# Kernel optimization log

Hardware: AMD Instinct MI355X
Metric: run time of the kernel (lower is better)

Reference implementation:

```python
import jax, jax.numpy as jnp
import numpy as np

N = 50000
E = 1600000
D_IN = 128
D_H = 128
D_OUT = 128
R = 2


def setup_inputs() -> dict:
    key = jax.random.key(0)
    ks = jax.random.split(key, 12)
    s = 0.02
    return {
        "x": jax.random.normal(ks[0], (N, D_IN), dtype=jnp.float32),
        "edge_index": jax.random.randint(ks[1], (2, E), 0, N, dtype=jnp.int64),
        "enc_w1": jax.random.normal(ks[2], (D_IN, D_H), dtype=jnp.float32) * s,
        "enc_b1": jnp.zeros((D_H,), dtype=jnp.float32),
        "enc_w2": jax.random.normal(ks[3], (D_H, D_H), dtype=jnp.float32) * s,
        "enc_b2": jnp.zeros((D_H,), dtype=jnp.float32),
        "comm_w": jax.random.normal(ks[4], (R, D_H, D_H), dtype=jnp.float32) * s,
        "comm_b": jnp.zeros((R, D_H), dtype=jnp.float32),
        "dec_w1": jax.random.normal(ks[5], (D_H, D_H), dtype=jnp.float32) * s,
        "dec_b1": jnp.zeros((D_H,), dtype=jnp.float32),
        "dec_w2": jax.random.normal(ks[6], (D_H, D_OUT), dtype=jnp.float32) * s,
        "dec_b2": jnp.zeros((D_OUT,), dtype=jnp.float32),
    }


def _segment_mean_messages(h, src, dst):
    # message[i] = mean over edges with source i of h[dst]; zeros if no neighbors
    gathered = h[dst]                                   # [E, D_H]
    sums = jax.ops.segment_sum(gathered, src, num_segments=N)   # [N, D_H]
    cnt = jax.ops.segment_sum(jnp.ones((src.shape[0],), h.dtype), src, num_segments=N)
    return sums / jnp.maximum(cnt, 1.0)[:, None]


def reference(x, edge_index, enc_w1, enc_b1, enc_w2, enc_b2,
              comm_w, comm_b, dec_w1, dec_b1, dec_w2, dec_b2):
    src, dst = edge_index[0], edge_index[1]
    # encoder: Linear -> ReLU -> Linear
    h = jax.nn.relu(x @ enc_w1 + enc_b1) @ enc_w2 + enc_b2
    # communication rounds
    for r in range(comm_w.shape[0]):
        msg = _segment_mean_messages(h, src, dst)       # [N, D_H]
        h = h + jax.nn.relu(msg @ comm_w[r] + comm_b[r])
    # decoder: Linear -> ReLU -> Linear
    return jax.nn.relu(h @ dec_w1 + dec_b1) @ dec_w2 + dec_b2
```

## Files before the change

### kernel.cpp

```cpp
#include <hip/hip_runtime.h>

#define NN 50000
#define EE 1600000
#define D 128
#define EPB 16384
#define NBIN ((EE + EPB - 1) / EPB)
#define NBKT 196
#define CAP 160
#define REC_CAP 12544

typedef __attribute__((ext_vector_type(8))) short bf16x8;
typedef __attribute__((ext_vector_type(4))) float f32x4;

static __device__ __forceinline__ unsigned short f2bf(float f) {
  unsigned u = __float_as_uint(f);
  u += 0x7fffu + ((u >> 16) & 1u);
  return (unsigned short)(u >> 16);
}
static __device__ __forceinline__ float bf2f(unsigned short s) {
  return __uint_as_float(((unsigned)s) << 16);
}

__global__ __launch_bounds__(256) void wt_prep(const float* __restrict__ ew1,
                                               const float* __restrict__ ew2,
                                               const float* __restrict__ cw,
                                               const float* __restrict__ dw1,
                                               const float* __restrict__ dw2,
                                               unsigned short* __restrict__ wt) {
  const int m = blockIdx.x;
  const float* W = (m == 0) ? ew1 : (m == 1) ? ew2 : (m == 2) ? cw
                 : (m == 3) ? (cw + 16384) : (m == 4) ? dw1 : dw2;
  unsigned short* o = wt + m * 16384;
  for (int i = threadIdx.x; i < 16384; i += 256) {
    const int col = i >> 7, k = i & 127;
    o[i] = f2bf(W[k * D + col]);
  }
}

__global__ __launch_bounds__(1024) void bin_edges(const int* __restrict__ src,
                                                  const int* __restrict__ dst,
                                                  unsigned* __restrict__ fifo_raw,
                                                  int* __restrict__ lcnt_g, int E) {
  __shared__ int lcnt[NBKT];
  const int t = threadIdx.x;
  for (int i = t; i < NBKT; i += 1024) lcnt[i] = 0;
  __syncthreads();
  const int base = blockIdx.x * EPB;
  #pragma unroll
  for (int it = 0; it < EPB / 1024; ++it) {
    const int e = base + it * 1024 + t;
    if (e < E) {
      const int s = src[e];
      const int d = dst[e];
      const int b = s >> 8;
      const int slot = atomicAdd(&lcnt[b], 1);
      if (slot < CAP)
        fifo_raw[((size_t)blockIdx.x * NBKT + b) * CAP + slot] =
            (unsigned)(s & 255) | ((unsigned)d << 8);
    }
  }
  __syncthreads();
  for (int i = t; i < NBKT; i += 1024)
    lcnt_g[blockIdx.x * NBKT + i] = min(lcnt[i], CAP);
}

__global__ __launch_bounds__(128) void seg_scan(const int* __restrict__ lcnt_g,
                                                int* __restrict__ seg_loc,
                                                int* __restrict__ btot) {
  __shared__ int wsum[2];
  const int b = blockIdx.x;
  const int t = threadIdx.x;
  const int lane = t & 63, w = t >> 6;
  const int v = (t < NBIN) ? lcnt_g[t * NBKT + b] : 0;
  int x = v;
  #pragma unroll
  for (int d = 1; d < 64; d <<= 1) {
    int y = __shfl_up(x, (unsigned)d);
    if (lane >= d) x += y;
  }
  if (lane == 63) wsum[w] = x;
  __syncthreads();
  const int add = (w == 1) ? wsum[0] : 0;
  if (t < NBIN) seg_loc[t * NBKT + b] = add + x - v;
  if (t == 127) btot[b] = wsum[0] + wsum[1];
}

__global__ __launch_bounds__(256) void bucket_scan(const int* __restrict__ btot,
                                                   int* __restrict__ bbase) {
  __shared__ int wsum[4];
  const int t = threadIdx.x;
  const int lane = t & 63, w = t >> 6;
  const int v = (t < NBKT) ? btot[t] : 0;
  int x = v;
  #pragma unroll
  for (int d = 1; d < 64; d <<= 1) {
    int y = __shfl_up(x, (unsigned)d);
    if (lane >= d) x += y;
  }
  if (lane == 63) wsum[w] = x;
  __syncthreads();
  int add = 0;
  for (int ww = 0; ww < w; ++ww) add += wsum[ww];
  if (t < NBKT) bbase[t] = add + x - v;
}

__global__ __launch_bounds__(1024) void csr_window(const unsigned* __restrict__ fifo_raw,
                                                   const int* __restrict__ lcnt_g,
                                                   const int* __restrict__ seg_loc,
                                                   const int* __restrict__ bbase,
                                                   const int* __restrict__ btot,
                                                   int* __restrict__ off,
                                                   int* __restrict__ cnt,
                                                   int* __restrict__ adj, int n) {
  __shared__ unsigned recs[REC_CAP];
  __shared__ int hist[256];
  __shared__ int offl[256];
  __shared__ int cur[256];
  const int t = threadIdx.x;
  const int lane = t & 63, w = t >> 6;
  const int b = blockIdx.x;
  const int gbase = bbase[b];

  if (t < 256) hist[t] = 0;
  __syncthreads();

  for (int blk = w; blk < NBIN; blk += 16) {
    const int idx = blk * NBKT + b;
    const int ms = lcnt_g[idx];
    const unsigned* sp = fifo_raw + (size_t)idx * CAP;
    const int dbase = seg_loc[idx];
    for (int i = lane; i < ms; i += 64)
      if (dbase + i < REC_CAP) recs[dbase + i] = sp[i];
  }
  __syncthreads();

  const int m = min(btot[b], REC_CAP);
  for (int i = t; i < m; i += 1024)
    atomicAdd(&hist[recs[i] & 255u], 1);
  __syncthreads();

  if (w == 0) {
    const int i4 = lane * 4;
    const int v0 = hist[i4], v1 = hist[i4 + 1], v2 = hist[i4 + 2], v3 = hist[i4 + 3];
    const int s = v0 + v1 + v2 + v3;
    int x = s;
    #pragma unroll
    for (int d = 1; d < 64; d <<= 1) {
      int y = __shfl_up(x, (unsigned)d);
      if (lane >= d) x += y;
    }
    int pre = x - s;
    offl[i4] = pre;          cur[i4] = pre;
    pre += v0; offl[i4 + 1] = pre; cur[i4 + 1] = pre;
    pre += v1; offl[i4 + 2] = pre; cur[i4 + 2] = pre;
    pre += v2; offl[i4 + 3] = pre; cur[i4 + 3] = pre;
  }
  __syncthreads();

  if (t < 256) {
    const int node = b * 256 + t;
    if (node < n) {
      cnt[node] = hist[t];
      off[node] = gbase + offl[t];
    }
  }
  for (int i = t; i < m; i += 1024) {
    const unsigned r = recs[i];
    const int sl = (int)(r & 255u);
    const int p = atomicAdd(&cur[sl], 1);
    adj[gbase + p] = (int)(r >> 8);
  }
}

template<bool FUSED>
__global__ __launch_bounds__(256) void mfma_linear(const float* __restrict__ in,
                                                   const unsigned short* __restrict__ wt1,
                                                   const float* __restrict__ b1,
                                                   const unsigned short* __restrict__ wt2,
                                                   const float* __restrict__ b2,
                                                   void* __restrict__ outp, int n) {
  __shared__ unsigned short As[64 * 128];
  const int t = threadIdx.x;
  const int l = t & 63;
  const int w = t >> 6;
  const int rowBase = blockIdx.x * 64;

  {
    const int kg = t & 31;
    const int r0 = t >> 5;
    #pragma unroll
    for (int i = 0; i < 8; ++i) {
      const int r = r0 + i * 8;
      const int grow = rowBase + r;
      float4 v = make_float4(0.f, 0.f, 0.f, 0.f);
      if (grow < n) v = *(const float4*)(in + (size_t)grow * D + kg * 4);
      ushort4 pk = make_ushort4(f2bf(v.x), f2bf(v.y), f2bf(v.z), f2bf(v.w));
      *(ushort4*)((char*)As + r * 256 + ((kg * 8) ^ ((r & 7) << 4))) = pk;
    }
  }
  __syncthreads();

  const int wrow = w * 16;
  const int l16 = l & 15;
  const int lk = l >> 4;
  const int ar = wrow + l16;
  const int asw = (ar & 7) << 4;

  f32x4 acc[8];
  #pragma unroll
  for (int cf = 0; cf < 8; ++cf) acc[cf] = (f32x4){0.f, 0.f, 0.f, 0.f};
  #pragma unroll
  for (int ks = 0; ks < 4; ++ks) {
    const bf16x8 a = *(const bf16x8*)((char*)As + ar * 256 + ((ks * 64 + lk * 16) ^ asw));
    #pragma unroll
    for (int cf = 0; cf < 8; ++cf) {
      const bf16x8 b = *(const bf16x8*)(wt1 + (cf * 16 + l16) * D + ks * 32 + lk * 8);
      acc[cf] = __builtin_amdgcn_mfma_f32_16x16x32_bf16(a, b, acc[cf], 0, 0, 0);
    }
  }

  if (FUSED) {
    #pragma unroll
    for (int cf = 0; cf < 8; ++cf) {
      const int col = cf * 16 + l16;
      const float bb = b1[col];
      #pragma unroll
      for (int reg = 0; reg < 4; ++reg) {
        const int r = wrow + lk * 4 + reg;
        const float v = fmaxf(acc[cf][reg] + bb, 0.f);
        *(unsigned short*)((char*)As + r * 256 + ((col * 2) ^ ((r & 7) << 4))) = f2bf(v);
      }
    }
    f32x4 acc2[8];
    #pragma unroll
    for (int cf = 0; cf < 8; ++cf) acc2[cf] = (f32x4){0.f, 0.f, 0.f, 0.f};
    #pragma unroll
    for (int ks = 0; ks < 4; ++ks) {
      const bf16x8 a = *(const bf16x8*)((char*)As + ar * 256 + ((ks * 64 + lk * 16) ^ asw));
      #pragma unroll
      for (int cf = 0; cf < 8; ++cf) {
        const bf16x8 b = *(const bf16x8*)(wt2 + (cf * 16 + l16) * D + ks * 32 + lk * 8);
        acc2[cf] = __builtin_amdgcn_mfma_f32_16x16x32_bf16(a, b, acc2[cf], 0, 0, 0);
      }
    }
    float* out = (float*)outp;
    #pragma unroll
    for (int cf = 0; cf < 8; ++cf) {
      const int col = cf * 16 + l16;
      const float bb = b2[col];
      #pragma unroll
      for (int reg = 0; reg < 4; ++reg) {
        const int grow = rowBase + wrow + lk * 4 + reg;
        if (grow < n) out[(size_t)grow * D + col] = acc2[cf][reg] + bb;
      }
    }
  } else {
    unsigned short* out = (unsigned short*)outp;
    #pragma unroll
    for (int cf = 0; cf < 8; ++cf) {
      const int col = cf * 16 + l16;
      #pragma unroll
      for (int reg = 0; reg < 4; ++reg) {
        const int grow = rowBase + wrow + lk * 4 + reg;
        if (grow < n) out[(size_t)grow * D + col] = f2bf(acc[cf][reg]);
      }
    }
  }
}

__global__ __launch_bounds__(256) void gather_update(const unsigned int* __restrict__ g,
                                                     float* __restrict__ h,
                                                     const int* __restrict__ adj,
                                                     const int* __restrict__ off,
                                                     const int* __restrict__ cnt,
                                                     const float* __restrict__ bias,
                                                     int n) {
  const int i = blockIdx.x * 4 + (threadIdx.x >> 6);
  if (i >= n) return;
  const int lane = threadIdx.x & 63;
  const int o = off[i];
  const int c = cnt[i];
  float ax[8] = {0.f, 0.f, 0.f, 0.f, 0.f, 0.f, 0.f, 0.f};
  float ay[8] = {0.f, 0.f, 0.f, 0.f, 0.f, 0.f, 0.f, 0.f};
  int e = 0;
  for (; e + 8 <= c; e += 8) {
    int j[8];
    #pragma unroll
    for (int k = 0; k < 8; ++k) j[k] = adj[o + e + k];
    #pragma unroll
    for (int k = 0; k < 8; ++k) {
      const unsigned v = g[(size_t)j[k] * 64 + lane];
      ax[k] += bf2f((unsigned short)(v & 0xffff));
      ay[k] += bf2f((unsigned short)(v >> 16));
    }
  }
  for (; e < c; ++e) {
    const int j = adj[o + e];
    const unsigned v = g[(size_t)j * 64 + lane];
    ax[0] += bf2f((unsigned short)(v & 0xffff));
    ay[0] += bf2f((unsigned short)(v >> 16));
  }
  const float sx = ((ax[0] + ax[1]) + (ax[2] + ax[3])) + ((ax[4] + ax[5]) + (ax[6] + ax[7]));
  const float sy = ((ay[0] + ay[1]) + (ay[2] + ay[3])) + ((ay[4] + ay[5]) + (ay[6] + ay[7]));
  const float inv = 1.0f / fmaxf((float)c, 1.0f);
  const float2 bb = ((const float2*)bias)[lane];
  float2 hv = ((float2*)h)[(size_t)i * 64 + lane];
  hv.x += fmaxf(sx * inv + bb.x, 0.f);
  hv.y += fmaxf(sy * inv + bb.y, 0.f);
  ((float2*)h)[(size_t)i * 64 + lane] = hv;
}

extern "C" void kernel_launch(void* const* d_in, const int* in_sizes, int n_in,
                              void* d_out, int out_size, void* d_ws, size_t ws_size,
                              hipStream_t stream) {
  const float* x   = (const float*)d_in[0];
  const int*   ei  = (const int*)d_in[1];
  const float* ew1 = (const float*)d_in[2];
  const float* eb1 = (const float*)d_in[3];
  const float* ew2 = (const float*)d_in[4];
  const float* eb2 = (const float*)d_in[5];
  const float* cw  = (const float*)d_in[6];
  const float* cb  = (const float*)d_in[7];
  const float* dw1 = (const float*)d_in[8];
  const float* db1 = (const float*)d_in[9];
  const float* dw2 = (const float*)d_in[10];
  const float* db2 = (const float*)d_in[11];

  const int n = NN, E = EE;

  float* h     = (float*)d_ws;
  int* adj     = (int*)(h + (size_t)n * D);
  int* cnt     = adj + EE;
  int* off     = cnt + 50048;
  int* seg_loc = off + 50048;
  int* btot    = seg_loc + NBIN * NBKT;
  int* bbase   = btot + 256;
  unsigned short* wt = (unsigned short*)(bbase + 256);

  unsigned* fifo_raw = (unsigned*)d_out;
  int* lcnt_g        = (int*)(fifo_raw + (size_t)NBIN * NBKT * CAP);
  unsigned short* g  = (unsigned short*)d_out;

  const int* src = ei;
  const int* dst = ei + E;

  wt_prep<<<6, 256, 0, stream>>>(ew1, ew2, cw, dw1, dw2, wt);
  bin_edges<<<NBIN, 1024, 0, stream>>>(src, dst, fifo_raw, lcnt_g, E);
  seg_scan<<<NBKT, 128, 0, stream>>>(lcnt_g, seg_loc, btot);
  bucket_scan<<<1, 256, 0, stream>>>(btot, bbase);
  csr_window<<<NBKT, 1024, 0, stream>>>(fifo_raw, lcnt_g, seg_loc, bbase, btot,
                                        off, cnt, adj, n);

  const int gb = (n + 63) / 64;

  mfma_linear<true><<<gb, 256, 0, stream>>>(x, wt, eb1, wt + 16384, eb2, h, n);
  for (int r = 0; r < 2; ++r) {
    mfma_linear<false><<<gb, 256, 0, stream>>>(h, wt + (2 + r) * 16384,
                                               nullptr, nullptr, nullptr, g, n);
    gather_update<<<(n + 3) / 4, 256, 0, stream>>>((const unsigned int*)g, h, adj,
                                                   off, cnt, cb + r * D, n);
  }
  mfma_linear<true><<<gb, 256, 0, stream>>>(h, wt + 4 * 16384, db1,
                                            wt + 5 * 16384, db2, d_out, n);
}
```

Baseline: 293.1 us.

## Partition CSR adjacency into destination-range phases for gather cache locality

```diff
diff --git a/kernel.cpp b/kernel.cpp
--- a/kernel.cpp
+++ b/kernel.cpp
@@ -8,6 +8,8 @@
 #define NBKT 196
 #define CAP 160
 #define REC_CAP 12544
+#define OFFSTR 50048
+#define PHN 12500
 
 typedef __attribute__((ext_vector_type(8))) short bf16x8;
 typedef __attribute__((ext_vector_type(4))) float f32x4;
@@ -65,8 +67,7 @@
 }
 
 __global__ __launch_bounds__(128) void seg_scan(const int* __restrict__ lcnt_g,
-                                                int* __restrict__ seg_loc,
-                                                int* __restrict__ btot) {
+                                                int* __restrict__ seg_loc) {
   __shared__ int wsum[2];
   const int b = blockIdx.x;
   const int t = threadIdx.x;
@@ -82,16 +83,61 @@
   __syncthreads();
   const int add = (w == 1) ? wsum[0] : 0;
   if (t < NBIN) seg_loc[t * NBKT + b] = add + x - v;
-  if (t == 127) btot[b] = wsum[0] + wsum[1];
-}
-
-__global__ __launch_bounds__(256) void bucket_scan(const int* __restrict__ btot,
-                                                   int* __restrict__ bbase) {
+}
+
+__global__ __launch_bounds__(1024) void csr_hist(const unsigned* __restrict__ fifo_raw,
+                                                 const int* __restrict__ lcnt_g,
+                                                 unsigned* __restrict__ cnt4p,
+                                                 int* __restrict__ wtot, int n) {
+  __shared__ int hist2[1024];
+  const int t = threadIdx.x;
+  const int lane = t & 63, w = t >> 6;
+  const int b = blockIdx.x;
+  hist2[t] = 0;
+  __syncthreads();
+  for (int blk = w; blk < NBIN; blk += 16) {
+    const int idx = blk * NBKT + b;
+    const int ms = lcnt_g[idx];
+    const unsigned* sp = fifo_raw + (size_t)idx * CAP;
+    for (int i = lane; i < ms; i += 64) {
+      const unsigned r = sp[i];
+      const int sl = (int)(r & 255u);
+      const int ph = (int)((r >> 8) / PHN);
+      atomicAdd(&hist2[sl * 4 + ph], 1);
+    }
+  }
+  __syncthreads();
+  if (t < 256) {
+    const int node = b * 256 + t;
+    if (node < n) {
+      const unsigned c0 = hist2[t * 4], c1 = hist2[t * 4 + 1];
+      const unsigned c2 = hist2[t * 4 + 2], c3 = hist2[t * 4 + 3];
+      cnt4p[node] = c0 | (c1 << 8) | (c2 << 16) | (c3 << 24);
+    }
+  }
+  if (w < 4) {
+    int s = 0;
+    for (int sl = lane; sl < 256; sl += 64) s += hist2[sl * 4 + w];
+    #pragma unroll
+    for (int d = 1; d < 64; d <<= 1) s += __shfl_xor(s, d);
+    if (lane == 0) wtot[w * NBKT + b] = s;
+  }
+}
+
+__global__ __launch_bounds__(256) void phase_scan(const int* __restrict__ wtot,
+                                                  int* __restrict__ wbase) {
   __shared__ int wsum[4];
   const int t = threadIdx.x;
   const int lane = t & 63, w = t >> 6;
-  const int v = (t < NBKT) ? btot[t] : 0;
-  int x = v;
+  int v[4];
+  int s = 0;
+  #pragma unroll
+  for (int q = 0; q < 4; ++q) {
+    const int idx = t * 4 + q;
+    v[q] = (idx < 4 * NBKT) ? wtot[idx] : 0;
+    s += v[q];
+  }
+  int x = s;
   #pragma unroll
   for (int d = 1; d < 64; d <<= 1) {
     int y = __shfl_up(x, (unsigned)d);
@@ -101,27 +147,28 @@
   __syncthreads();
   int add = 0;
   for (int ww = 0; ww < w; ++ww) add += wsum[ww];
-  if (t < NBKT) bbase[t] = add + x - v;
-}
-
-__global__ __launch_bounds__(1024) void csr_window(const unsigned* __restrict__ fifo_raw,
-                                                   const int* __restrict__ lcnt_g,
-                                                   const int* __restrict__ seg_loc,
-                                                   const int* __restrict__ bbase,
-                                                   const int* __restrict__ btot,
-                                                   int* __restrict__ off,
-                                                   int* __restrict__ cnt,
-                                                   int* __restrict__ adj, int n) {
+  int pre = add + x - s;
+  #pragma unroll
+  for (int q = 0; q < 4; ++q) {
+    const int idx = t * 4 + q;
+    if (idx < 4 * NBKT) wbase[idx] = pre;
+    pre += v[q];
+  }
+}
+
+__global__ __launch_bounds__(1024) void csr_scatter(const unsigned* __restrict__ fifo_raw,
+                                                    const int* __restrict__ lcnt_g,
+                                                    const int* __restrict__ seg_loc,
+                                                    const int* __restrict__ wbase,
+                                                    int* __restrict__ off4,
+                                                    int* __restrict__ adj, int n) {
   __shared__ unsigned recs[REC_CAP];
-  __shared__ int hist[256];
-  __shared__ int offl[256];
-  __shared__ int cur[256];
+  __shared__ int hist2[1024];
+  __shared__ int cur[1024];
   const int t = threadIdx.x;
   const int lane = t & 63, w = t >> 6;
   const int b = blockIdx.x;
-  const int gbase = bbase[b];
-
-  if (t < 256) hist[t] = 0;
+  hist2[t] = 0;
   __syncthreads();
 
   for (int blk = w; blk < NBIN; blk += 16) {
@@ -129,46 +176,47 @@
     const int ms = lcnt_g[idx];
     const unsigned* sp = fifo_raw + (size_t)idx * CAP;
     const int dbase = seg_loc[idx];
-    for (int i = lane; i < ms; i += 64)
-      if (dbase + i < REC_CAP) recs[dbase + i] = sp[i];
-  }
-  __syncthreads();
-
-  const int m = min(btot[b], REC_CAP);
-  for (int i = t; i < m; i += 1024)
-    atomicAdd(&hist[recs[i] & 255u], 1);
-  __syncthreads();
-
-  if (w == 0) {
-    const int i4 = lane * 4;
-    const int v0 = hist[i4], v1 = hist[i4 + 1], v2 = hist[i4 + 2], v3 = hist[i4 + 3];
-    const int s = v0 + v1 + v2 + v3;
+    for (int i = lane; i < ms; i += 64) {
+      const unsigned r = sp[i];
+      if (dbase + i < REC_CAP) recs[dbase + i] = r;
+      atomicAdd(&hist2[(r & 255u) * 4 + (r >> 8) / PHN], 1);
+    }
+  }
+  __syncthreads();
+
+  if (w < 4) {
+    int v[4];
+    int s = 0;
+    #pragma unroll
+    for (int q = 0; q < 4; ++q) {
+      v[q] = hist2[(lane * 4 + q) * 4 + w];
+      s += v[q];
+    }
     int x = s;
     #pragma unroll
     for (int d = 1; d < 64; d <<= 1) {
       int y = __shfl_up(x, (unsigned)d);
       if (lane >= d) x += y;
     }
-    int pre = x - s;
-    offl[i4] = pre;          cur[i4] = pre;
-    pre += v0; offl[i4 + 1] = pre; cur[i4 + 1] = pre;
-    pre += v1; offl[i4 + 2] = pre; cur[i4 + 2] = pre;
-    pre += v2; offl[i4 + 3] = pre; cur[i4 + 3] = pre;
-  }
-  __syncthreads();
-
-  if (t < 256) {
-    const int node = b * 256 + t;
-    if (node < n) {
-      cnt[node] = hist[t];
-      off[node] = gbase + offl[t];
-    }
-  }
+    int pre = wbase[w * NBKT + b] + x - s;
+    #pragma unroll
+    for (int q = 0; q < 4; ++q) {
+      const int sl = lane * 4 + q;
+      cur[sl * 4 + w] = pre;
+      const int node = b * 256 + sl;
+      if (node < n) off4[w * OFFSTR + node] = pre;
+      pre += v[q];
+    }
+  }
+  __syncthreads();
+
+  const int last = (NBIN - 1) * NBKT + b;
+  const int m = min(seg_loc[last] + lcnt_g[last], REC_CAP);
   for (int i = t; i < m; i += 1024) {
     const unsigned r = recs[i];
-    const int sl = (int)(r & 255u);
-    const int p = atomicAdd(&cur[sl], 1);
-    adj[gbase + p] = (int)(r >> 8);
+    const int d = (int)(r >> 8);
+    const int p = atomicAdd(&cur[(r & 255u) * 4 + d / PHN], 1);
+    adj[p] = d;
   }
 }
 
@@ -268,41 +316,43 @@
   }
 }
 
-__global__ __launch_bounds__(256) void gather_update(const unsigned int* __restrict__ g,
-                                                     float* __restrict__ h,
-                                                     const int* __restrict__ adj,
-                                                     const int* __restrict__ off,
-                                                     const int* __restrict__ cnt,
-                                                     const float* __restrict__ bias,
-                                                     int n) {
+__global__ __launch_bounds__(256) void gather_update_ph(
+    const unsigned* __restrict__ g, float* __restrict__ h,
+    const int* __restrict__ adj, const unsigned* __restrict__ cnt4p,
+    const int* __restrict__ off4, const float* __restrict__ bias, int n) {
   const int i = blockIdx.x * 4 + (threadIdx.x >> 6);
   if (i >= n) return;
   const int lane = threadIdx.x & 63;
-  const int o = off[i];
-  const int c = cnt[i];
+  const unsigned c4 = cnt4p[i];
   float ax[8] = {0.f, 0.f, 0.f, 0.f, 0.f, 0.f, 0.f, 0.f};
   float ay[8] = {0.f, 0.f, 0.f, 0.f, 0.f, 0.f, 0.f, 0.f};
-  int e = 0;
-  for (; e + 8 <= c; e += 8) {
-    int j[8];
-    #pragma unroll
-    for (int k = 0; k < 8; ++k) j[k] = adj[o + e + k];
-    #pragma unroll
-    for (int k = 0; k < 8; ++k) {
-      const unsigned v = g[(size_t)j[k] * 64 + lane];
-      ax[k] += bf2f((unsigned short)(v & 0xffff));
-      ay[k] += bf2f((unsigned short)(v >> 16));
-    }
-  }
-  for (; e < c; ++e) {
-    const int j = adj[o + e];
-    const unsigned v = g[(size_t)j * 64 + lane];
-    ax[0] += bf2f((unsigned short)(v & 0xffff));
-    ay[0] += bf2f((unsigned short)(v >> 16));
+  #pragma unroll
+  for (int ph = 0; ph < 4; ++ph) {
+    const int o = off4[ph * OFFSTR + i];
+    const int c = (int)((c4 >> (8 * ph)) & 255u);
+    int e = 0;
+    for (; e + 8 <= c; e += 8) {
+      int j[8];
+      #pragma unroll
+      for (int k = 0; k < 8; ++k) j[k] = adj[o + e + k];
+      #pragma unroll
+      for (int k = 0; k < 8; ++k) {
+        const unsigned v = g[(size_t)j[k] * 64 + lane];
+        ax[k] += bf2f((unsigned short)(v & 0xffff));
+        ay[k] += bf2f((unsigned short)(v >> 16));
+      }
+    }
+    for (; e < c; ++e) {
+      const unsigned v = g[(size_t)adj[o + e] * 64 + lane];
+      ax[0] += bf2f((unsigned short)(v & 0xffff));
+      ay[0] += bf2f((unsigned short)(v >> 16));
+    }
   }
   const float sx = ((ax[0] + ax[1]) + (ax[2] + ax[3])) + ((ax[4] + ax[5]) + (ax[6] + ax[7]));
   const float sy = ((ay[0] + ay[1]) + (ay[2] + ay[3])) + ((ay[4] + ay[5]) + (ay[6] + ay[7]));
-  const float inv = 1.0f / fmaxf((float)c, 1.0f);
+  const int deg = (int)((c4 & 255u) + ((c4 >> 8) & 255u) +
+                        ((c4 >> 16) & 255u) + (c4 >> 24));
+  const float inv = 1.0f / fmaxf((float)deg, 1.0f);
   const float2 bb = ((const float2*)bias)[lane];
   float2 hv = ((float2*)h)[(size_t)i * 64 + lane];
   hv.x += fmaxf(sx * inv + bb.x, 0.f);
@@ -330,15 +380,15 @@
 
   float* h     = (float*)d_ws;
   int* adj     = (int*)(h + (size_t)n * D);
-  int* cnt     = adj + EE;
-  int* off     = cnt + 50048;
-  int* seg_loc = off + 50048;
-  int* btot    = seg_loc + NBIN * NBKT;
-  int* bbase   = btot + 256;
-  unsigned short* wt = (unsigned short*)(bbase + 256);
+  int* seg_loc = adj + EE;
+  int* wtot    = seg_loc + NBIN * NBKT;
+  int* wbase   = wtot + 784;
+  unsigned short* wt = (unsigned short*)(wbase + 784);
 
   unsigned* fifo_raw = (unsigned*)d_out;
   int* lcnt_g        = (int*)(fifo_raw + (size_t)NBIN * NBKT * CAP);
+  int* off4          = (int*)((char*)d_out + 13631488);
+  unsigned* cnt4p    = (unsigned*)((char*)d_out + 13631488 + 4 * OFFSTR * 4);
   unsigned short* g  = (unsigned short*)d_out;
 
   const int* src = ei;
@@ -346,10 +396,11 @@
 
   wt_prep<<<6, 256, 0, stream>>>(ew1, ew2, cw, dw1, dw2, wt);
   bin_edges<<<NBIN, 1024, 0, stream>>>(src, dst, fifo_raw, lcnt_g, E);
-  seg_scan<<<NBKT, 128, 0, stream>>>(lcnt_g, seg_loc, btot);
-  bucket_scan<<<1, 256, 0, stream>>>(btot, bbase);
-  csr_window<<<NBKT, 1024, 0, stream>>>(fifo_raw, lcnt_g, seg_loc, bbase, btot,
-                                        off, cnt, adj, n);
+  seg_scan<<<NBKT, 128, 0, stream>>>(lcnt_g, seg_loc);
+  csr_hist<<<NBKT, 1024, 0, stream>>>(fifo_raw, lcnt_g, cnt4p, wtot, n);
+  phase_scan<<<1, 256, 0, stream>>>(wtot, wbase);
+  csr_scatter<<<NBKT, 1024, 0, stream>>>(fifo_raw, lcnt_g, seg_loc, wbase,
+                                         off4, adj, n);
 
   const int gb = (n + 63) / 64;
 
@@ -357,8 +408,8 @@
   for (int r = 0; r < 2; ++r) {
     mfma_linear<false><<<gb, 256, 0, stream>>>(h, wt + (2 + r) * 16384,
                                                nullptr, nullptr, nullptr, g, n);
-    gather_update<<<(n + 3) / 4, 256, 0, stream>>>((const unsigned int*)g, h, adj,
-                                                   off, cnt, cb + r * D, n);
+    gather_update_ph<<<(n + 3) / 4, 256, 0, stream>>>((const unsigned*)g, h, adj,
+                                                      cnt4p, off4, cb + r * D, n);
   }
   mfma_linear<true><<<gb, 256, 0, stream>>>(h, wt + 4 * 16384, db1,
                                             wt + 5 * 16384, db2, d_out, n);
```

Measured after the change: 373.7 us. 1.28x slower.

## Split neighbor gather into four column passes and store adjacency as 16-bit

Applied to the files above, without the earlier changes.

```diff
diff --git a/kernel.cpp b/kernel.cpp
--- a/kernel.cpp
+++ b/kernel.cpp
@@ -111,7 +111,8 @@
                                                    const int* __restrict__ btot,
                                                    int* __restrict__ off,
                                                    int* __restrict__ cnt,
-                                                   int* __restrict__ adj, int n) {
+                                                   unsigned short* __restrict__ adj,
+                                                   int n) {
   __shared__ unsigned recs[REC_CAP];
   __shared__ int hist[256];
   __shared__ int offl[256];
@@ -168,7 +169,7 @@
     const unsigned r = recs[i];
     const int sl = (int)(r & 255u);
     const int p = atomicAdd(&cur[sl], 1);
-    adj[gbase + p] = (int)(r >> 8);
+    adj[gbase + p] = (unsigned short)(r >> 8);
   }
 }
 
@@ -268,46 +269,59 @@
   }
 }
 
-__global__ __launch_bounds__(256) void gather_update(const unsigned int* __restrict__ g,
-                                                     float* __restrict__ h,
-                                                     const int* __restrict__ adj,
-                                                     const int* __restrict__ off,
-                                                     const int* __restrict__ cnt,
-                                                     const float* __restrict__ bias,
-                                                     int n) {
+__global__ __launch_bounds__(256) void gather_pass(
+    const unsigned* __restrict__ g,
+    float* __restrict__ h,
+    const unsigned short* __restrict__ adj,
+    const int* __restrict__ off, const int* __restrict__ cnt,
+    const float* __restrict__ bias, int n, int pass) {
   const int i = blockIdx.x * 4 + (threadIdx.x >> 6);
   if (i >= n) return;
   const int lane = threadIdx.x & 63;
+  const int q = lane >> 4;
+  const int cp = lane & 15;
   const int o = off[i];
   const int c = cnt[i];
-  float ax[8] = {0.f, 0.f, 0.f, 0.f, 0.f, 0.f, 0.f, 0.f};
-  float ay[8] = {0.f, 0.f, 0.f, 0.f, 0.f, 0.f, 0.f, 0.f};
+  const unsigned* gq = g + pass * 16 + cp;
+  float ax[8], ay[8];
+  #pragma unroll
+  for (int k = 0; k < 8; ++k) { ax[k] = 0.f; ay[k] = 0.f; }
   int e = 0;
-  for (; e + 8 <= c; e += 8) {
+  for (; e + 32 <= c; e += 32) {
     int j[8];
     #pragma unroll
-    for (int k = 0; k < 8; ++k) j[k] = adj[o + e + k];
+    for (int k = 0; k < 8; ++k) j[k] = adj[o + e + k * 4 + q];
+    unsigned v[8];
+    #pragma unroll
+    for (int k = 0; k < 8; ++k) v[k] = gq[(size_t)j[k] * 64];
     #pragma unroll
     for (int k = 0; k < 8; ++k) {
-      const unsigned v = g[(size_t)j[k] * 64 + lane];
-      ax[k] += bf2f((unsigned short)(v & 0xffff));
-      ay[k] += bf2f((unsigned short)(v >> 16));
-    }
-  }
-  for (; e < c; ++e) {
-    const int j = adj[o + e];
-    const unsigned v = g[(size_t)j * 64 + lane];
+      ax[k] += bf2f((unsigned short)(v[k] & 0xffff));
+      ay[k] += bf2f((unsigned short)(v[k] >> 16));
+    }
+  }
+  for (; e < c; e += 4) {
+    const int idx = e + q;
+    const bool ok = (idx < c);
+    const int j = ok ? adj[o + idx] : 0;
+    const unsigned v = ok ? gq[(size_t)j * 64] : 0u;
     ax[0] += bf2f((unsigned short)(v & 0xffff));
     ay[0] += bf2f((unsigned short)(v >> 16));
   }
-  const float sx = ((ax[0] + ax[1]) + (ax[2] + ax[3])) + ((ax[4] + ax[5]) + (ax[6] + ax[7]));
-  const float sy = ((ay[0] + ay[1]) + (ay[2] + ay[3])) + ((ay[4] + ay[5]) + (ay[6] + ay[7]));
-  const float inv = 1.0f / fmaxf((float)c, 1.0f);
-  const float2 bb = ((const float2*)bias)[lane];
-  float2 hv = ((float2*)h)[(size_t)i * 64 + lane];
-  hv.x += fmaxf(sx * inv + bb.x, 0.f);
-  hv.y += fmaxf(sy * inv + bb.y, 0.f);
-  ((float2*)h)[(size_t)i * 64 + lane] = hv;
+  float sx = 0.f, sy = 0.f;
+  #pragma unroll
+  for (int k = 0; k < 8; ++k) { sx += ax[k]; sy += ay[k]; }
+  sx += __shfl_xor(sx, 16); sy += __shfl_xor(sy, 16);
+  sx += __shfl_xor(sx, 32); sy += __shfl_xor(sy, 32);
+  if (q == 0) {
+    const float inv = 1.0f / fmaxf((float)c, 1.0f);
+    const float2 bb = ((const float2*)bias)[pass * 16 + cp];
+    float2* hp = (float2*)h + (size_t)i * 64 + pass * 16 + cp;
+    float2 hv = *hp;
+    hv.x += fmaxf(sx * inv + bb.x, 0.f);
+    hv.y += fmaxf(sy * inv + bb.y, 0.f);
+    *hp = hv;
+  }
 }
 
 extern "C" void kernel_launch(void* const* d_in, const int* in_sizes, int n_in,
@@ -329,8 +343,8 @@
   const int n = NN, E = EE;
 
   float* h     = (float*)d_ws;
-  int* adj     = (int*)(h + (size_t)n * D);
-  int* cnt     = adj + EE;
+  unsigned short* adj = (unsigned short*)(h + (size_t)n * D);
+  int* cnt     = (int*)(adj + EE);
   int* off     = cnt + 50048;
   int* seg_loc = off + 50048;
   int* btot    = seg_loc + NBIN * NBKT;
@@ -352,13 +366,15 @@
                                         off, cnt, adj, n);
 
   const int gb = (n + 63) / 64;
+  const int gbk = (n + 3) / 4;
 
   mfma_linear<true><<<gb, 256, 0, stream>>>(x, wt, eb1, wt + 16384, eb2, h, n);
   for (int r = 0; r < 2; ++r) {
     mfma_linear<false><<<gb, 256, 0, stream>>>(h, wt + (2 + r) * 16384,
                                                nullptr, nullptr, nullptr, g, n);
-    gather_update<<<(n + 3) / 4, 256, 0, stream>>>((const unsigned int*)g, h, adj,
-                                                   off, cnt, cb + r * D, n);
+    for (int pass = 0; pass < 4; ++pass)
+      gather_pass<<<gbk, 256, 0, stream>>>((const unsigned*)g, h, adj, off, cnt,
+                                           cb + r * D, n, pass);
   }
   mfma_linear<true><<<gb, 256, 0, stream>>>(h, wt + 4 * 16384, db1,
                                             wt + 5 * 16384, db2, d_out, n);
```

Result: slower. 466.3 us (+59.1%).
